# Kernel tuning notes

Hardware: AMD Instinct MI355X
Metric: run time of the kernel (lower is better)

The kernel has to match this reference:

```python
import jax, jax.numpy as jnp
import numpy as np

BS, N, N_HEAD, F_IN, F_OUT = 8, 1024, 8, 256, 64
NEG_SLOPE = 0.2


def setup_inputs() -> dict:
    key = jax.random.key(0)
    k_h, k_adj, k_w, k_src, k_dst = jax.random.split(key, 5)
    h = jax.random.normal(k_h, (BS, N, F_IN), dtype=jnp.float32)
    adj = jax.random.randint(k_adj, (BS, N, N), 0, 2) > 0  # bool adjacency
    # xavier_uniform-style params
    def xavier(k, shape, fan_in, fan_out):
        limit = float(np.sqrt(6.0 / (fan_in + fan_out)))
        return jax.random.uniform(k, shape, jnp.float32, -limit, limit)
    w = xavier(k_w, (N_HEAD, F_IN, F_OUT), F_IN, F_OUT)
    a_src = xavier(k_src, (N_HEAD, F_OUT, 1), F_OUT, 1)
    a_dst = xavier(k_dst, (N_HEAD, F_OUT, 1), F_OUT, 1)
    bias = jnp.zeros((F_OUT,), dtype=jnp.float32)
    return {"h": h, "adj": adj, "w": w, "a_src": a_src, "a_dst": a_dst, "bias": bias}


def reference(h, adj, w, a_src, a_dst, bias):
    # h: [bs, n, f_in], w: [n_head, f_in, f_out]
    h_prime = jnp.einsum('bnf,hfo->bhno', h, w)            # [bs, h, n, f_out]
    t = jnp.tanh(h_prime)
    attn_src = jnp.einsum('bhno,ho->bhn', t, a_src[..., 0])  # [bs, h, n]
    attn_dst = jnp.einsum('bhno,ho->bhn', t, a_dst[..., 0])  # [bs, h, n]
    attn = attn_src[:, :, :, None] + attn_dst[:, :, None, :]  # [bs, h, n, n]
    attn = jnp.where(attn >= 0, attn, NEG_SLOPE * attn)       # leaky_relu(0.2)
    n = adj.shape[-1]
    mask = ~(adj[:, None, :, :] | jnp.eye(n, dtype=bool))     # [bs, 1->h, n, n]
    attn = jnp.where(mask, -jnp.inf, attn)
    attn = jax.nn.softmax(attn, axis=-1)                      # diag always valid
    out = jnp.einsum('bhnm,bhmo->bhno', attn, h_prime)
    return out + bias
```

## Files before the change

### kernel.cpp

```cpp
#include <hip/hip_runtime.h>
#include <math.h>

#define BS 8
#define NPTS 1024
#define NH 8
#define FIN 256
#define FOUT 64

typedef __attribute__((ext_vector_type(8))) short s8v;
typedef __attribute__((ext_vector_type(8))) _Float16 h8v;
typedef __attribute__((ext_vector_type(2))) __fp16 fp16x2;
typedef __attribute__((ext_vector_type(4))) float f4v;
typedef unsigned long long u64;

__device__ __forceinline__ unsigned short f2bf(float f) {
  unsigned u = __float_as_uint(f);
  return (unsigned short)((u + 0x7fffu + ((u >> 16) & 1u)) >> 16);
}
__device__ __forceinline__ float bf2f(unsigned short s) {
  return __uint_as_float(((unsigned)s) << 16);
}
__device__ __forceinline__ float fast_tanh(float x) {
  float e = __expf(2.f * x);
  return 1.f - 2.f / (e + 1.f);
}
__device__ __forceinline__ float hw_exp2(float x) {
  float r;
  asm("v_exp_f32 %0, %1" : "=v"(r) : "v"(x));
  return r;
}

__device__ __forceinline__ void gl_lds16(const void* g, void* l) {
  __builtin_amdgcn_global_load_lds(
      (const __attribute__((address_space(1))) unsigned*)g,
      (__attribute__((address_space(3))) unsigned*)l, 16, 0, 0);
}

__global__ __launch_bounds__(256) void prep_kernel(
    const void* __restrict__ adjv, const float* __restrict__ w,
    u64* __restrict__ abits,
    unsigned short* __restrict__ wT_hi, unsigned short* __restrict__ wT_lo)
{
  const int blk = blockIdx.x;
  const int t = threadIdx.x;
  if (blk < 2048) {
    __shared__ int badsh;
    if (t == 0) badsh = 0;
    __syncthreads();
    if (((const unsigned*)adjv)[t] > 1u) badsh = 1;
    __syncthreads();
    const int lane = t & 63;
    const int gw = blk * 4 + (t >> 6);
    const int b = gw >> 10, i = gw & 1023;
    const int m16 = lane & 15, g = lane >> 4;
    u64 words[4];
    if (badsh == 0) {
      const int4* row4 = (const int4*)((const int*)adjv + ((size_t)b * NPTS + i) * NPTS);
      int4 av[4];
      av[0] = row4[lane]; av[1] = row4[lane + 64];
      av[2] = row4[lane + 128]; av[3] = row4[lane + 192];
#pragma unroll
      for (int ci = 0; ci < 4; ++ci) {
        unsigned n = (unsigned)(av[ci].x != 0) | ((unsigned)(av[ci].y != 0) << 1) |
                     ((unsigned)(av[ci].z != 0) << 2) | ((unsigned)(av[ci].w != 0) << 3);
        unsigned d = (unsigned)(i - (ci * 256 + 4 * lane));
        if (d < 4u) n |= 1u << d;
        u64 val = (u64)n << (4 * m16);
#pragma unroll
        for (int msk = 1; msk <= 8; msk <<= 1)
          val |= (u64)__shfl_xor(val, msk, 64);
        words[ci] = val;
      }
    } else {
      const unsigned* rowB = (const unsigned*)((const unsigned char*)adjv + ((size_t)b * NPTS + i) * NPTS);
      unsigned av[4];
      av[0] = rowB[lane]; av[1] = rowB[lane + 64];
      av[2] = rowB[lane + 128]; av[3] = rowB[lane + 192];
#pragma unroll
      for (int ci = 0; ci < 4; ++ci) {
        unsigned v = av[ci];
        unsigned n = ((v & 0xffu) ? 1u : 0u) | (((v >> 8) & 0xffu) ? 2u : 0u) |
                     (((v >> 16) & 0xffu) ? 4u : 0u) | ((v >> 24) ? 8u : 0u);
        unsigned d = (unsigned)(i - (ci * 256 + 4 * lane));
        if (d < 4u) n |= 1u << d;
        u64 val = (u64)n << (4 * m16);
#pragma unroll
        for (int msk = 1; msk <= 8; msk <<= 1)
          val |= (u64)__shfl_xor(val, msk, 64);
        words[ci] = val;
      }
    }
    if (m16 == 0) {
#pragma unroll
      for (int ci = 0; ci < 4; ++ci)
        abits[((size_t)b * NPTS + i) * 16 + ci * 4 + g] = words[ci];
    }
  } else {
    const int bb = blk - 2048;
    const int hh = bb >> 3, ks = bb & 7;
    const int o = t & 63, kq = t >> 6;
#pragma unroll
    for (int e = 0; e < 8; ++e) {
      int k = ks * 32 + kq * 8 + e;
      float v = w[((size_t)hh * FIN + k) * FOUT + o];
      unsigned short hi = f2bf(v);
      wT_hi[((size_t)hh * FOUT + o) * FIN + k] = hi;
      wT_lo[((size_t)hh * FOUT + o) * FIN + k] = f2bf(v - bf2f(hi));
    }
  }
}

union ProjSmem {
  unsigned short Bbuf[3][4096];
  float tile[64][65];
};

__global__ __launch_bounds__(256, 4) void proj_kernel(
    const float* __restrict__ h,
    const unsigned short* __restrict__ wT_hi, const unsigned short* __restrict__ wT_lo,
    const float* __restrict__ a_src, const float* __restrict__ a_dst,
    unsigned short* __restrict__ hfrag,
    float* __restrict__ srcb, float* __restrict__ dstb)
{
  __shared__ ProjSmem sm;

  const int t = threadIdx.x;
  const int lane = t & 63;
  const int wv = t >> 6;
  const int blk = blockIdx.x;
  const int it = blk & 15;
  const int hh = (blk >> 4) & 7;
  const int b  = blk >> 7;
  const int i0 = it * 64;
  const int bh = b * NH + hh;
  const int l15 = lane & 15;
  const int g4  = lane >> 4;
  const int koff = g4 * 8;

  const int o_t  = t >> 2;
  const int gsrc = (t & 3) ^ ((o_t >> 1) & 3);
  const unsigned short* gB_hi = wT_hi + ((size_t)(hh * FOUT + o_t)) * FIN + gsrc * 8;
  const unsigned short* gB_lo = wT_lo + ((size_t)(hh * FOUT + o_t)) * FIN + gsrc * 8;

  const float* arow = h + ((size_t)(b * NPTS + i0 + wv * 16 + l15)) * FIN + koff;

  const int sw = (l15 >> 1) & 3;
  int roff[4];
#pragma unroll
  for (int nt = 0; nt < 4; ++nt)
    roff[nt] = (nt * 16 + l15) * 32 + (g4 ^ sw) * 8;

  float4 hA[3][2];
  gl_lds16(gB_hi, &sm.Bbuf[0][wv * 512]);
  gl_lds16(gB_lo, &sm.Bbuf[0][2048 + wv * 512]);
  hA[0][0] = *(const float4*)(arow);
  hA[0][1] = *(const float4*)(arow + 4);
  __builtin_amdgcn_sched_barrier(0);
  gl_lds16(gB_hi + 32, &sm.Bbuf[1][wv * 512]);
  gl_lds16(gB_lo + 32, &sm.Bbuf[1][2048 + wv * 512]);
  hA[1][0] = *(const float4*)(arow + 32);
  hA[1][1] = *(const float4*)(arow + 36);

  f4v acc[4];
#pragma unroll
  for (int nt = 0; nt < 4; ++nt) acc[nt] = 0.0f;

#pragma unroll
  for (int k0 = 0; k0 < 8; ++k0) {
    if (k0 == 7) asm volatile("s_waitcnt vmcnt(0)" ::: "memory");
    else         asm volatile("s_waitcnt vmcnt(4)" ::: "memory");
    __builtin_amdgcn_sched_barrier(0);
    __builtin_amdgcn_s_barrier();
    __builtin_amdgcn_sched_barrier(0);

    if (k0 < 6) {
      const int nb = (k0 + 2) % 3;
      gl_lds16(gB_hi + (k0 + 2) * 32, &sm.Bbuf[nb][wv * 512]);
      gl_lds16(gB_lo + (k0 + 2) * 32, &sm.Bbuf[nb][2048 + wv * 512]);
      hA[nb][0] = *(const float4*)(arow + (k0 + 2) * 32);
      hA[nb][1] = *(const float4*)(arow + (k0 + 2) * 32 + 4);
    }
    __builtin_amdgcn_sched_barrier(0);

    const int cb = k0 % 3;
    float av[8] = {hA[cb][0].x, hA[cb][0].y, hA[cb][0].z, hA[cb][0].w,
                   hA[cb][1].x, hA[cb][1].y, hA[cb][1].z, hA[cb][1].w};
    s8v Ah, Al;
#pragma unroll
    for (int e = 0; e < 8; ++e) {
      unsigned u = __float_as_uint(av[e]);
      float r = av[e] - __uint_as_float(u & 0xffff0000u);
      Ah[e] = (short)(unsigned short)(u >> 16);
      Al[e] = (short)(unsigned short)(__float_as_uint(r) >> 16);
    }

    const unsigned short* fb = &sm.Bbuf[cb][0];
#pragma unroll
    for (int nt = 0; nt < 4; ++nt) {
      s8v Bh = *(const s8v*)(fb + roff[nt]);
      s8v Bl = *(const s8v*)(fb + 2048 + roff[nt]);
      acc[nt] = __builtin_amdgcn_mfma_f32_16x16x32_bf16(Ah, Bh, acc[nt], 0, 0, 0);
      acc[nt] = __builtin_amdgcn_mfma_f32_16x16x32_bf16(Al, Bh, acc[nt], 0, 0, 0);
      acc[nt] = __builtin_amdgcn_mfma_f32_16x16x32_bf16(Ah, Bl, acc[nt], 0, 0, 0);
    }
  }
  __syncthreads();

  float a_s[4], a_d[4];
#pragma unroll
  for (int nt = 0; nt < 4; ++nt) {
    a_s[nt] = a_src[hh * FOUT + nt * 16 + l15];
    a_d[nt] = a_dst[hh * FOUT + nt * 16 + l15];
  }
#pragma unroll
  for (int qq = 0; qq < 4; ++qq) {
    float ps = 0.f, pd = 0.f;
#pragma unroll
    for (int nt = 0; nt < 4; ++nt) {
      float tv = fast_tanh(acc[nt][qq]);
      ps = fmaf(tv, a_s[nt], ps);
      pd = fmaf(tv, a_d[nt], pd);
    }
#pragma unroll
    for (int m = 8; m >= 1; m >>= 1) {
      ps += __shfl_xor(ps, m, 64);
      pd += __shfl_xor(pd, m, 64);
    }
    if (l15 == 0) {
      int row = i0 + wv * 16 + g4 * 4 + qq;
      srcb[(size_t)bh * NPTS + row] = ps;
      dstb[(size_t)bh * NPTS + row] = pd;
    }
  }

#pragma unroll
  for (int nt = 0; nt < 4; ++nt)
#pragma unroll
    for (int qq = 0; qq < 4; ++qq)
      sm.tile[wv * 16 + g4 * 4 + qq][nt * 16 + l15] = acc[nt][qq];
  __syncthreads();

  const int cbase = t >> 6;
#pragma unroll
  for (int ci = 0; ci < 2; ++ci) {
    int cc = cbase + ci * 4;
    int ks = cc >> 2, nt2 = cc & 3;
    int jb = ks * 32 + ((lane >> 4) * 8);
    int ob = nt2 * 16 + l15;
    h8v v;
#pragma unroll
    for (int e = 0; e < 8; ++e) v[e] = (_Float16)sm.tile[jb + e][ob];
    *(h8v*)(hfrag + (((size_t)(bh * 16 + it) * 8 + cc) * 64 + lane) * 8) = v;
  }
}

__global__ __launch_bounds__(256, 4) void attn_kernel(
    const u64* __restrict__ abits,
    const unsigned short* __restrict__ hfrag,
    const float* __restrict__ srcb, const float* __restrict__ dstb,
    const float* __restrict__ bias, float* __restrict__ out)
{
  __shared__ float e1sh[NPTS];
  __shared__ float e2sh[NPTS];
  __shared__ float wred[4];
  __shared__ uint2 mlut[16];
  __shared__ unsigned short frag[2][4096];

  const int t = threadIdx.x;
  const int lane = t & 63;
  const int wv = t >> 6;
  const int blk = blockIdx.x;
  const int it = blk & 15;
  const int hh = (blk >> 4) & 7;
  const int b  = blk >> 7;
  const int i0 = it * 64;
  const int bh = b * NH + hh;
  const int l15 = lane & 15;
  const int koff = (lane >> 4) * 8;
  const int rowA = i0 + wv * 16 + l15;

  const uint4* fgb = (const uint4*)hfrag + (size_t)bh * 16 * 512;
  const u64* abrow = abits + ((size_t)b * NPTS + rowA) * 16;

  uint4 s0 = fgb[t];
  uint4 s1 = fgb[t + 256];
  u64 ab_cur = abrow[0];
  const float src_r = srcb[(size_t)bh * NPTS + rowA];
  float4 dv = ((const float4*)(dstb + (size_t)bh * NPTS))[t];

  if (t < 16) {
    unsigned m = t;
    mlut[t] = make_uint2(
        ((m & 1u) ? 0xFFFFu : 0u) | (((m >> 1) & 1u) ? 0xFFFF0000u : 0u),
        (((m >> 2) & 1u) ? 0xFFFFu : 0u) | (((m >> 3) & 1u) ? 0xFFFF0000u : 0u));
  }

  const float L2E = 1.44269504f;
  {
    float4 e1, e2;
    e1.x = hw_exp2(dv.x * L2E);          e1.y = hw_exp2(dv.y * L2E);
    e1.z = hw_exp2(dv.z * L2E);          e1.w = hw_exp2(dv.w * L2E);
    e2.x = hw_exp2(dv.x * (0.2f * L2E)); e2.y = hw_exp2(dv.y * (0.2f * L2E));
    e2.z = hw_exp2(dv.z * (0.2f * L2E)); e2.w = hw_exp2(dv.w * (0.2f * L2E));
    ((float4*)e1sh)[t] = e1;
    ((float4*)e2sh)[t] = e2;
  }
  float lm = fmaxf(fmaxf(dv.x, dv.y), fmaxf(dv.z, dv.w));
#pragma unroll
  for (int m = 32; m >= 1; m >>= 1) lm = fmaxf(lm, __shfl_xor(lm, m, 64));
  if (lane == 0) wred[wv] = lm;
  __syncthreads();
  const float M = fmaxf(fmaxf(wred[0], wred[1]), fmaxf(wred[2], wred[3]));
  const float xm = src_r + M;
  const float m_row = fmaxf(xm, 0.2f * xm);
  const float Ai = hw_exp2((src_r - m_row) * L2E);
  const float Bi = hw_exp2((0.2f * src_r - m_row) * L2E);

  ((uint4*)&frag[0][0])[t]       = s0;
  ((uint4*)&frag[0][0])[t + 256] = s1;
  __syncthreads();

  h8v ones;
#pragma unroll
  for (int e = 0; e < 8; ++e) ones[e] = (_Float16)1.0f;

  f4v acc[4], acc_l;
#pragma unroll
  for (int nt = 0; nt < 4; ++nt) acc[nt] = 0.0f;
  acc_l = 0.0f;

#pragma unroll 2
  for (int jt = 0; jt < 16; ++jt) {
    const int buf = jt & 1;
    uint4 n0, n1; u64 ab_nxt;
    if (jt < 15) {
      const uint4* fgn = fgb + (size_t)(jt + 1) * 512;
      n0 = fgn[t];
      n1 = fgn[t + 256];
      ab_nxt = abrow[jt + 1];
    }
    __builtin_amdgcn_sched_barrier(0);

    const int jb = jt * 64 + koff;
    float4 ea0 = *(const float4*)&e1sh[jb];
    float4 ea1 = *(const float4*)&e1sh[jb + 4];
    float4 eb0 = *(const float4*)&e2sh[jb];
    float4 eb1 = *(const float4*)&e2sh[jb + 4];
    float4 ec0 = *(const float4*)&e1sh[jb + 32];
    float4 ec1 = *(const float4*)&e1sh[jb + 36];
    float4 ed0 = *(const float4*)&e2sh[jb + 32];
    float4 ed1 = *(const float4*)&e2sh[jb + 36];
    float p0[8] = {
      fmaxf(Ai * ea0.x, Bi * eb0.x), fmaxf(Ai * ea0.y, Bi * eb0.y),
      fmaxf(Ai * ea0.z, Bi * eb0.z), fmaxf(Ai * ea0.w, Bi * eb0.w),
      fmaxf(Ai * ea1.x, Bi * eb1.x), fmaxf(Ai * ea1.y, Bi * eb1.y),
      fmaxf(Ai * ea1.z, Bi * eb1.z), fmaxf(Ai * ea1.w, Bi * eb1.w)};
    float p1[8] = {
      fmaxf(Ai * ec0.x, Bi * ed0.x), fmaxf(Ai * ec0.y, Bi * ed0.y),
      fmaxf(Ai * ec0.z, Bi * ed0.z), fmaxf(Ai * ec0.w, Bi * ed0.w),
      fmaxf(Ai * ec1.x, Bi * ed1.x), fmaxf(Ai * ec1.y, Bi * ed1.y),
      fmaxf(Ai * ec1.z, Bi * ed1.z), fmaxf(Ai * ec1.w, Bi * ed1.w)};
    const unsigned w0 = (unsigned)(ab_cur) >> koff;
    const unsigned w1 = (unsigned)(ab_cur >> 32) >> koff;
    union { fp16x2 q[4]; unsigned u[4]; h8v v; } ua, ub;
    ua.q[0] = __builtin_amdgcn_cvt_pkrtz(p0[0], p0[1]);
    ua.q[1] = __builtin_amdgcn_cvt_pkrtz(p0[2], p0[3]);
    ua.q[2] = __builtin_amdgcn_cvt_pkrtz(p0[4], p0[5]);
    ua.q[3] = __builtin_amdgcn_cvt_pkrtz(p0[6], p0[7]);
    ub.q[0] = __builtin_amdgcn_cvt_pkrtz(p1[0], p1[1]);
    ub.q[1] = __builtin_amdgcn_cvt_pkrtz(p1[2], p1[3]);
    ub.q[2] = __builtin_amdgcn_cvt_pkrtz(p1[4], p1[5]);
    ub.q[3] = __builtin_amdgcn_cvt_pkrtz(p1[6], p1[7]);
    {
      uint2 ma0 = mlut[w0 & 15], ma1 = mlut[(w0 >> 4) & 15];
      uint2 mb0 = mlut[w1 & 15], mb1 = mlut[(w1 >> 4) & 15];
      ua.u[0] &= ma0.x; ua.u[1] &= ma0.y; ua.u[2] &= ma1.x; ua.u[3] &= ma1.y;
      ub.u[0] &= mb0.x; ub.u[1] &= mb0.y; ub.u[2] &= mb1.x; ub.u[3] &= mb1.y;
    }
    h8v pa0 = ua.v;
    h8v pa1 = ub.v;

    __builtin_amdgcn_s_setprio(1);
#pragma unroll
    for (int nt = 0; nt < 4; ++nt) {
      h8v B0 = *(const h8v*)&frag[buf][(nt * 64 + lane) * 8];
      acc[nt] = __builtin_amdgcn_mfma_f32_16x16x32_f16(pa0, B0, acc[nt], 0, 0, 0);
    }
    acc_l = __builtin_amdgcn_mfma_f32_16x16x32_f16(pa0, ones, acc_l, 0, 0, 0);
#pragma unroll
    for (int nt = 0; nt < 4; ++nt) {
      h8v B1 = *(const h8v*)&frag[buf][((4 + nt) * 64 + lane) * 8];
      acc[nt] = __builtin_amdgcn_mfma_f32_16x16x32_f16(pa1, B1, acc[nt], 0, 0, 0);
    }
    acc_l = __builtin_amdgcn_mfma_f32_16x16x32_f16(pa1, ones, acc_l, 0, 0, 0);
    __builtin_amdgcn_s_setprio(0);

    if (jt < 15) {
      ((uint4*)&frag[buf ^ 1][0])[t]       = n0;
      ((uint4*)&frag[buf ^ 1][0])[t + 256] = n1;
      ab_cur = ab_nxt;
    }
    __syncthreads();
  }

  float bias4[4];
#pragma unroll
  for (int nt = 0; nt < 4; ++nt) bias4[nt] = bias[nt * 16 + l15];

#pragma unroll
  for (int qq = 0; qq < 4; ++qq) {
    float linv = 1.0f / acc_l[qq];
    int rowq = i0 + wv * 16 + (lane >> 4) * 4 + qq;
    size_t ob = ((size_t)bh * NPTS + rowq) * FOUT;
#pragma unroll
    for (int nt = 0; nt < 4; ++nt)
      out[ob + nt * 16 + l15] = acc[nt][qq] * linv + bias4[nt];
  }
}

extern "C" void kernel_launch(void* const* d_in, const int* in_sizes, int n_in,
                              void* d_out, int out_size, void* d_ws, size_t ws_size,
                              hipStream_t stream)
{
  const float* h     = (const float*)d_in[0];
  const void*  adj   = d_in[1];
  const float* w     = (const float*)d_in[2];
  const float* a_src = (const float*)d_in[3];
  const float* a_dst = (const float*)d_in[4];
  const float* bias  = (const float*)d_in[5];
  float* out = (float*)d_out;

  char* p = (char*)d_ws;
  float* srcb = (float*)p;                      p += (size_t)BS * NH * NPTS * 4;
  float* dstb = (float*)p;                      p += (size_t)BS * NH * NPTS * 4;
  unsigned short* wT_hi = (unsigned short*)p;   p += (size_t)NH * FOUT * FIN * 2;
  unsigned short* wT_lo = (unsigned short*)p;   p += (size_t)NH * FOUT * FIN * 2;
  u64* abits = (u64*)p;                         p += (size_t)BS * NPTS * 16 * 8;
  unsigned short* hfrag = (unsigned short*)p;

  prep_kernel<<<dim3(2112), dim3(256), 0, stream>>>(adj, w, abits, wT_hi, wT_lo);
  proj_kernel<<<dim3(1024), dim3(256), 0, stream>>>(
      h, wT_hi, wT_lo, a_src, a_dst, hfrag, srcb, dstb);
  attn_kernel<<<dim3(1024), dim3(256), 0, stream>>>(
      abits, hfrag, srcb, dstb, bias, out);
}
```

Measured before the change: 47.74 us.

## Move adjacency bit-packing into projection kernel, split weight conversion out

```diff
diff --git a/kernel.cpp b/kernel.cpp
--- a/kernel.cpp
+++ b/kernel.cpp
@@ -36,19 +36,48 @@
       (__attribute__((address_space(3))) unsigned*)l, 16, 0, 0);
 }
 
-__global__ __launch_bounds__(256) void prep_kernel(
-    const void* __restrict__ adjv, const float* __restrict__ w,
-    u64* __restrict__ abits,
+__global__ __launch_bounds__(256) void wsplit_kernel(
+    const float* __restrict__ w,
     unsigned short* __restrict__ wT_hi, unsigned short* __restrict__ wT_lo)
 {
   const int blk = blockIdx.x;
   const int t = threadIdx.x;
-  if (blk < 2048) {
-    __shared__ int badsh;
-    if (t == 0) badsh = 0;
+  const int hh = blk >> 3, ks = blk & 7;
+  const int o = t & 63, kq = t >> 6;
+#pragma unroll
+  for (int e = 0; e < 8; ++e) {
+    int k = ks * 32 + kq * 8 + e;
+    float v = w[((size_t)hh * FIN + k) * FOUT + o];
+    unsigned short hi = f2bf(v);
+    wT_hi[((size_t)hh * FOUT + o) * FIN + k] = hi;
+    wT_lo[((size_t)hh * FOUT + o) * FIN + k] = f2bf(v - bf2f(hi));
+  }
+}
+
+union ProjSmem {
+  unsigned short Bbuf[3][4096];
+  float tile[64][65];
+  int badsh;
+};
+
+__global__ __launch_bounds__(256, 4) void projpack_kernel(
+    const float* __restrict__ h, const void* __restrict__ adjv,
+    const unsigned short* __restrict__ wT_hi, const unsigned short* __restrict__ wT_lo,
+    const float* __restrict__ a_src, const float* __restrict__ a_dst,
+    u64* __restrict__ abits, unsigned short* __restrict__ hfrag,
+    float* __restrict__ srcb, float* __restrict__ dstb)
+{
+  __shared__ ProjSmem sm;
+  const int t = threadIdx.x;
+  const int blkAll = blockIdx.x;
+
+  if (blkAll >= 1024) {
+    const int blk = blkAll - 1024;
+    if (t == 0) sm.badsh = 0;
     __syncthreads();
-    if (((const unsigned*)adjv)[t] > 1u) badsh = 1;
+    if (((const unsigned*)adjv)[t] > 1u) sm.badsh = 1;
     __syncthreads();
+    const int badsh = sm.badsh;
     const int lane = t & 63;
     const int gw = blk * 4 + (t >> 6);
     const int b = gw >> 10, i = gw & 1023;
@@ -95,39 +124,12 @@
       for (int ci = 0; ci < 4; ++ci)
         abits[((size_t)b * NPTS + i) * 16 + ci * 4 + g] = words[ci];
     }
-  } else {
-    const int bb = blk - 2048;
-    const int hh = bb >> 3, ks = bb & 7;
-    const int o = t & 63, kq = t >> 6;
-#pragma unroll
-    for (int e = 0; e < 8; ++e) {
-      int k = ks * 32 + kq * 8 + e;
-      float v = w[((size_t)hh * FIN + k) * FOUT + o];
-      unsigned short hi = f2bf(v);
-      wT_hi[((size_t)hh * FOUT + o) * FIN + k] = hi;
-      wT_lo[((size_t)hh * FOUT + o) * FIN + k] = f2bf(v - bf2f(hi));
-    }
-  }
-}
-
-union ProjSmem {
-  unsigned short Bbuf[3][4096];
-  float tile[64][65];
-};
-
-__global__ __launch_bounds__(256, 4) void proj_kernel(
-    const float* __restrict__ h,
-    const unsigned short* __restrict__ wT_hi, const unsigned short* __restrict__ wT_lo,
-    const float* __restrict__ a_src, const float* __restrict__ a_dst,
-    unsigned short* __restrict__ hfrag,
-    float* __restrict__ srcb, float* __restrict__ dstb)
-{
-  __shared__ ProjSmem sm;
-
-  const int t = threadIdx.x;
+    return;
+  }
+
+  const int blk = blkAll;
   const int lane = t & 63;
   const int wv = t >> 6;
-  const int blk = blockIdx.x;
   const int it = blk & 15;
   const int hh = (blk >> 4) & 7;
   const int b  = blk >> 7;
@@ -438,9 +440,9 @@
   u64* abits = (u64*)p;                         p += (size_t)BS * NPTS * 16 * 8;
   unsigned short* hfrag = (unsigned short*)p;
 
-  prep_kernel<<<dim3(2112), dim3(256), 0, stream>>>(adj, w, abits, wT_hi, wT_lo);
-  proj_kernel<<<dim3(1024), dim3(256), 0, stream>>>(
-      h, wT_hi, wT_lo, a_src, a_dst, hfrag, srcb, dstb);
+  wsplit_kernel<<<dim3(64), dim3(256), 0, stream>>>(w, wT_hi, wT_lo);
+  projpack_kernel<<<dim3(3072), dim3(256), 0, stream>>>(
+      h, adj, wT_hi, wT_lo, a_src, a_dst, abits, hfrag, srcb, dstb);
   attn_kernel<<<dim3(1024), dim3(256), 0, stream>>>(
       abits, hfrag, srcb, dstb, bias, out);
 }
```

New measurement: 48.12 us. About the same (+0.8%).
